# Kernel tuning notes

Hardware: AMD Instinct MI355X
Metric: run time of the kernel (lower is better)

## Reference

```python
import jax, jax.numpy as jnp
import numpy as np

DEPTH = 11  # tree depth -> depth+1 routing steps, n_nodes = 2**(DEPTH+1)-1 = 4095


def setup_inputs() -> dict:
    key = jax.random.key(0)
    k1, k2, k3 = jax.random.split(key, 3)
    B, D_in, D_out = 8192, 2048, 2048
    n_nodes = 2 ** (DEPTH + 1) - 1
    x = jax.random.normal(k1, (B, D_in), dtype=jnp.float32)
    # nn.Linear(input_width, n_nodes, bias=False).weight : (n_nodes, D_in)
    W_in = jax.random.normal(k2, (n_nodes, D_in), dtype=jnp.float32) / np.sqrt(D_in).astype(np.float32)
    # nn.Linear(n_nodes, output_width, bias=False).weight : (D_out, n_nodes)
    W_out = jax.random.normal(k3, (D_out, n_nodes), dtype=jnp.float32) / np.sqrt(n_nodes).astype(np.float32)
    return {"x": x, "W_in": W_in, "W_out": W_out}


def reference(x, W_in, W_out):
    B = x.shape[0]
    # Torch loop recomputes linear_in(x) every step; the result is identical each
    # iteration, so compute the (B, n_nodes) logits once and gather per depth step.
    logits_all = x @ W_in.T  # (B, n_nodes)

    def step(cur, _):
        # gather the logit of each sample's current tree node
        score = jnp.take_along_axis(logits_all, cur[:, None], axis=1)[:, 0]  # (B,)
        nxt = cur * 2 + (score >= 0).astype(jnp.int32) + 1  # left/right child
        return nxt, (cur, score)

    init = jnp.zeros((B,), dtype=jnp.int32)
    _, (nodes, scores) = jax.lax.scan(step, init, None, length=DEPTH + 1)
    nodes = nodes.T    # (B, depth+1) visited node ids
    scores = scores.T  # (B, depth+1) selected logits

    mlp1 = jax.nn.gelu(scores, approximate=False)  # exact GELU, matches nn.GELU
    # Conditional output projection: only the depth+1 visited columns of W_out
    # contribute per sample (FFF / conditional-MoE semantics).
    W_sel = W_out.T[nodes]  # (B, depth+1, D_out)
    return jnp.einsum('bd,bdo->bo', mlp1, W_sel)
```

## Files before the change

### kernel.cpp

```cpp
#include <hip/hip_runtime.h>
#include <math.h>

#define B_SZ     8192
#define D_IN     2048
#define D_OUT    2048
#define N_NODES  4095
#define STEPS    12
#define N_LEAVES 2048
#define N_SUB    512
#define CAP      64

__global__ __launch_bounds__(256) void transpose_wout(
    const float* __restrict__ W, float* __restrict__ Wt) {
  __shared__ float tile[64][65];
  const int bx = blockIdx.x;
  const int tid = threadIdx.x;
  const int col0 = (bx & 63) * 64;
  const int row0 = (bx >> 6) * 64;
  const int r  = tid >> 4;
  const int c4 = (tid & 15) * 4;

  #pragma unroll
  for (int i = 0; i < 4; ++i) {
    const int row = r + i * 16;
    const float* src = W + (size_t)(row0 + row) * N_NODES + col0 + c4;
    if (col0 + c4 + 3 < N_NODES) {
      const float4 v = *(const float4*)src;
      tile[c4 + 0][row] = v.x; tile[c4 + 1][row] = v.y;
      tile[c4 + 2][row] = v.z; tile[c4 + 3][row] = v.w;
    } else {
      #pragma unroll
      for (int k = 0; k < 4; ++k)
        tile[c4 + k][row] = (col0 + c4 + k < N_NODES) ? src[k] : 0.0f;
    }
  }
  __syncthreads();
  #pragma unroll
  for (int i = 0; i < 4; ++i) {
    const int rn = r + i * 16;
    const int node = col0 + rn;
    if (node < N_NODES) {
      float4 v;
      v.x = tile[rn][c4 + 0]; v.y = tile[rn][c4 + 1];
      v.z = tile[rn][c4 + 2]; v.w = tile[rn][c4 + 3];
      *(float4*)(Wt + (size_t)node * D_OUT + row0 + c4) = v;
    }
  }
}

__global__ __launch_bounds__(256) void route_kernel(
    const float* __restrict__ x, const float* __restrict__ W_in,
    int* __restrict__ cnt, int* __restrict__ bucket,
    float* __restrict__ gsc) {
  const int wave = (int)((blockIdx.x * (size_t)blockDim.x + threadIdx.x) >> 6);
  const int lane = threadIdx.x & 63;
  if (wave >= B_SZ) return;

  const float4* xr = (const float4*)(x + (size_t)wave * D_IN);
  float4 xv[8];
  #pragma unroll
  for (int i = 0; i < 8; ++i) xv[i] = xr[lane + i * 64];

  int cur = 0;
  #pragma unroll
  for (int d = 0; d < STEPS; ++d) {
    const float4* wr = (const float4*)(W_in + (size_t)cur * D_IN);
    float s = 0.0f;
    #pragma unroll
    for (int i = 0; i < 8; ++i) {
      const float4 w = wr[lane + i * 64];
      s += xv[i].x * w.x + xv[i].y * w.y + xv[i].z * w.z + xv[i].w * w.w;
    }
    #pragma unroll
    for (int off = 32; off > 0; off >>= 1) s += __shfl_xor(s, off);

    if (lane == 0) {
      gsc[wave * STEPS + d] = 0.5f * s * (1.0f + erff(s * 0.70710678118654752f));
      if (d == STEPS - 1) {
        const int leaf = cur - 2047;
        const int pos = atomicAdd(&cnt[leaf], 1);
        if (pos < CAP) bucket[leaf * CAP + pos] = wave;
      }
    }
    cur = cur * 2 + ((s >= 0.0f) ? 2 : 1);
  }
}

__global__ __launch_bounds__(64, 4) void out_kernel(
    const float* __restrict__ Wt, const int* __restrict__ cnt,
    const int* __restrict__ bucket, const float* __restrict__ gsc,
    float* __restrict__ out) {
  const int sub = blockIdx.x;
  const int col = blockIdx.y * 256 + threadIdx.x * 4;

  int anc[10];
  {
    int nd = 511 + sub;
    #pragma unroll
    for (int d = 9; d >= 0; --d) { anc[d] = nd; nd = (nd - 1) >> 1; }
  }
  const int p10a = 1023 + 2 * sub;
  const int leaf0n = 2047 + 4 * sub;

  float4 wa[10], wp[2], wl[4];
  #pragma unroll
  for (int d = 0; d < 10; ++d)
    wa[d] = *(const float4*)(Wt + (size_t)anc[d] * D_OUT + col);
  #pragma unroll
  for (int k = 0; k < 2; ++k)
    wp[k] = *(const float4*)(Wt + (size_t)(p10a + k) * D_OUT + col);
  #pragma unroll
  for (int k = 0; k < 4; ++k)
    wl[k] = *(const float4*)(Wt + (size_t)(leaf0n + k) * D_OUT + col);

  #pragma unroll
  for (int local = 0; local < 4; ++local) {
    const int leaf = 4 * sub + local;
    int n = cnt[leaf];
    if (n > CAP) n = CAP;
    const float4 w10 = wp[local >> 1];
    const float4 w11 = wl[local];
    for (int s = 0; s < n; ++s) {
      const int b = bucket[leaf * CAP + s];
      const float4* gp = (const float4*)(gsc + (size_t)b * STEPS);
      const float4 g0 = gp[0], g1 = gp[1], g2 = gp[2];
      float4 acc;
      acc.x = g0.x * wa[0].x; acc.y = g0.x * wa[0].y;
      acc.z = g0.x * wa[0].z; acc.w = g0.x * wa[0].w;
      acc.x += g0.y * wa[1].x; acc.y += g0.y * wa[1].y;
      acc.z += g0.y * wa[1].z; acc.w += g0.y * wa[1].w;
      acc.x += g0.z * wa[2].x; acc.y += g0.z * wa[2].y;
      acc.z += g0.z * wa[2].z; acc.w += g0.z * wa[2].w;
      acc.x += g0.w * wa[3].x; acc.y += g0.w * wa[3].y;
      acc.z += g0.w * wa[3].z; acc.w += g0.w * wa[3].w;
      acc.x += g1.x * wa[4].x; acc.y += g1.x * wa[4].y;
      acc.z += g1.x * wa[4].z; acc.w += g1.x * wa[4].w;
      acc.x += g1.y * wa[5].x; acc.y += g1.y * wa[5].y;
      acc.z += g1.y * wa[5].z; acc.w += g1.y * wa[5].w;
      acc.x += g1.z * wa[6].x; acc.y += g1.z * wa[6].y;
      acc.z += g1.z * wa[6].z; acc.w += g1.z * wa[6].w;
      acc.x += g1.w * wa[7].x; acc.y += g1.w * wa[7].y;
      acc.z += g1.w * wa[7].z; acc.w += g1.w * wa[7].w;
      acc.x += g2.x * wa[8].x; acc.y += g2.x * wa[8].y;
      acc.z += g2.x * wa[8].z; acc.w += g2.x * wa[8].w;
      acc.x += g2.y * wa[9].x; acc.y += g2.y * wa[9].y;
      acc.z += g2.y * wa[9].z; acc.w += g2.y * wa[9].w;
      acc.x += g2.z * w10.x;   acc.y += g2.z * w10.y;
      acc.z += g2.z * w10.z;   acc.w += g2.z * w10.w;
      acc.x += g2.w * w11.x;   acc.y += g2.w * w11.y;
      acc.z += g2.w * w11.z;   acc.w += g2.w * w11.w;
      *(float4*)(out + (size_t)b * D_OUT + col) = acc;
    }
  }
}

extern "C" void kernel_launch(void* const* d_in, const int* in_sizes, int n_in,
                              void* d_out, int out_size, void* d_ws, size_t ws_size,
                              hipStream_t stream) {
  const float* x     = (const float*)d_in[0];
  const float* W_in  = (const float*)d_in[1];
  const float* W_out = (const float*)d_in[2];
  float* out = (float*)d_out;

  char* p = (char*)d_ws;
  float* Wt     = (float*)p;  p += (size_t)N_NODES * D_OUT * sizeof(float);
  int*   cnt    = (int*)p;    p += (size_t)N_LEAVES * sizeof(int);
  int*   bucket = (int*)p;    p += (size_t)N_LEAVES * CAP * sizeof(int);
  float* gsc    = (float*)p;

  hipMemsetAsync(cnt, 0, (size_t)N_LEAVES * sizeof(int), stream);

  transpose_wout<<<dim3(2048), dim3(256), 0, stream>>>(W_out, Wt);

  route_kernel<<<dim3(B_SZ / 4), dim3(256), 0, stream>>>(
      x, W_in, cnt, bucket, gsc);

  out_kernel<<<dim3(N_SUB, 8), dim3(64), 0, stream>>>(
      Wt, cnt, bucket, gsc, out);
}
```

Baseline: 232.3 us.

## Fuse W_out transpose into routing kernel and prefetch both child rows

Merges the W_out transpose and the routing pass into one launch, with odd blocks transposing and even blocks routing, so the two independent memory-bound phases can overlap. Routing now loads both child rows of W_in one step ahead and computes both dot products, which removes the serialized load latency on the tree walk at the cost of doubling W_in reads and register pressure. Routing buffers the GELU scores and writes them as three float4 stores. The output kernel flattens the four leaf buckets into one loop, loading bucket ids cooperatively and software-pipelining the gsc loads two samples ahead.

```diff
diff --git a/kernel.cpp b/kernel.cpp
--- a/kernel.cpp
+++ b/kernel.cpp
@@ -10,88 +10,136 @@
 #define N_SUB    512
 #define CAP      64
 
-__global__ __launch_bounds__(256) void transpose_wout(
-    const float* __restrict__ W, float* __restrict__ Wt) {
-  __shared__ float tile[64][65];
-  const int bx = blockIdx.x;
-  const int tid = threadIdx.x;
-  const int col0 = (bx & 63) * 64;
-  const int row0 = (bx >> 6) * 64;
-  const int r  = tid >> 4;
-  const int c4 = (tid & 15) * 4;
-
-  #pragma unroll
-  for (int i = 0; i < 4; ++i) {
-    const int row = r + i * 16;
-    const float* src = W + (size_t)(row0 + row) * N_NODES + col0 + c4;
-    if (col0 + c4 + 3 < N_NODES) {
-      const float4 v = *(const float4*)src;
-      tile[c4 + 0][row] = v.x; tile[c4 + 1][row] = v.y;
-      tile[c4 + 2][row] = v.z; tile[c4 + 3][row] = v.w;
-    } else {
-      #pragma unroll
-      for (int k = 0; k < 4; ++k)
-        tile[c4 + k][row] = (col0 + c4 + k < N_NODES) ? src[k] : 0.0f;
-    }
-  }
-  __syncthreads();
-  #pragma unroll
-  for (int i = 0; i < 4; ++i) {
-    const int rn = r + i * 16;
-    const int node = col0 + rn;
-    if (node < N_NODES) {
-      float4 v;
-      v.x = tile[rn][c4 + 0]; v.y = tile[rn][c4 + 1];
-      v.z = tile[rn][c4 + 2]; v.w = tile[rn][c4 + 3];
-      *(float4*)(Wt + (size_t)node * D_OUT + row0 + c4) = v;
-    }
-  }
-}
-
-__global__ __launch_bounds__(256) void route_kernel(
+__global__ __launch_bounds__(256, 4) void route_tr_kernel(
     const float* __restrict__ x, const float* __restrict__ W_in,
+    const float* __restrict__ W_out, float* __restrict__ Wt,
     int* __restrict__ cnt, int* __restrict__ bucket,
     float* __restrict__ gsc) {
-  const int wave = (int)((blockIdx.x * (size_t)blockDim.x + threadIdx.x) >> 6);
-  const int lane = threadIdx.x & 63;
-  if (wave >= B_SZ) return;
+  __shared__ float tile[64][65];
+  const int tid = threadIdx.x;
+
+  if (blockIdx.x & 1) {
+    const int bx = blockIdx.x >> 1;
+    const int col0 = (bx & 63) * 64;
+    const int row0 = (bx >> 6) * 64;
+    const int r  = tid >> 4;
+    const int c4 = (tid & 15) * 4;
+    #pragma unroll
+    for (int i = 0; i < 4; ++i) {
+      const int row = r + i * 16;
+      const float* src = W_out + (size_t)(row0 + row) * N_NODES + col0 + c4;
+      if (col0 + c4 + 3 < N_NODES) {
+        const float4 v = *(const float4*)src;
+        tile[c4 + 0][row] = v.x; tile[c4 + 1][row] = v.y;
+        tile[c4 + 2][row] = v.z; tile[c4 + 3][row] = v.w;
+      } else {
+        #pragma unroll
+        for (int k = 0; k < 4; ++k)
+          tile[c4 + k][row] = (col0 + c4 + k < N_NODES) ? src[k] : 0.0f;
+      }
+    }
+    __syncthreads();
+    #pragma unroll
+    for (int i = 0; i < 4; ++i) {
+      const int rn = r + i * 16;
+      const int node = col0 + rn;
+      if (node < N_NODES) {
+        float4 v;
+        v.x = tile[rn][c4 + 0]; v.y = tile[rn][c4 + 1];
+        v.z = tile[rn][c4 + 2]; v.w = tile[rn][c4 + 3];
+        *(float4*)(Wt + (size_t)node * D_OUT + row0 + c4) = v;
+      }
+    }
+    return;
+  }
+
+  const int wave = (blockIdx.x >> 1) * 4 + (tid >> 6);
+  const int lane = tid & 63;
 
   const float4* xr = (const float4*)(x + (size_t)wave * D_IN);
   float4 xv[8];
   #pragma unroll
   for (int i = 0; i < 8; ++i) xv[i] = xr[lane + i * 64];
 
-  int cur = 0;
-  #pragma unroll
-  for (int d = 0; d < STEPS; ++d) {
-    const float4* wr = (const float4*)(W_in + (size_t)cur * D_IN);
-    float s = 0.0f;
+  float4 cl[8], cr[8];
+  {
+    const float4* p0 = (const float4*)W_in;
+    #pragma unroll
+    for (int i = 0; i < 8; ++i) cl[i] = p0[lane + i * 64];
+  }
+  float s = 0.0f;
+  #pragma unroll
+  for (int i = 0; i < 8; ++i)
+    s += xv[i].x * cl[i].x + xv[i].y * cl[i].y +
+         xv[i].z * cl[i].z + xv[i].w * cl[i].w;
+  {
+    const float4* p1 = (const float4*)(W_in + (size_t)1 * D_IN);
+    const float4* p2 = (const float4*)(W_in + (size_t)2 * D_IN);
+    #pragma unroll
+    for (int i = 0; i < 8; ++i) cl[i] = p1[lane + i * 64];
+    #pragma unroll
+    for (int i = 0; i < 8; ++i) cr[i] = p2[lane + i * 64];
+  }
+  #pragma unroll
+  for (int off = 32; off > 0; off >>= 1) s += __shfl_xor(s, off);
+
+  float gv[STEPS];
+  if (lane == 0) gv[0] = 0.5f * s * (1.0f + erff(s * 0.70710678118654752f));
+  int right = (s >= 0.0f) ? 1 : 0;
+  int cur = 1 + right;
+
+  #pragma unroll
+  for (int d = 1; d < STEPS; ++d) {
+    float sL = 0.0f, sR = 0.0f;
     #pragma unroll
     for (int i = 0; i < 8; ++i) {
-      const float4 w = wr[lane + i * 64];
-      s += xv[i].x * w.x + xv[i].y * w.y + xv[i].z * w.z + xv[i].w * w.w;
-    }
-    #pragma unroll
-    for (int off = 32; off > 0; off >>= 1) s += __shfl_xor(s, off);
-
+      sL += xv[i].x * cl[i].x + xv[i].y * cl[i].y +
+            xv[i].z * cl[i].z + xv[i].w * cl[i].w;
+      sR += xv[i].x * cr[i].x + xv[i].y * cr[i].y +
+            xv[i].z * cr[i].z + xv[i].w * cr[i].w;
+    }
+    const int curs = __builtin_amdgcn_readfirstlane(cur);
+    if (d < STEPS - 1) {
+      const float4* pl = (const float4*)(W_in + (size_t)(2 * curs + 1) * D_IN);
+      const float4* pr = (const float4*)(W_in + (size_t)(2 * curs + 2) * D_IN);
+      #pragma unroll
+      for (int i = 0; i < 8; ++i) cl[i] = pl[lane + i * 64];
+      #pragma unroll
+      for (int i = 0; i < 8; ++i) cr[i] = pr[lane + i * 64];
+    }
+    #pragma unroll
+    for (int off = 32; off > 0; off >>= 1) {
+      sL += __shfl_xor(sL, off);
+      sR += __shfl_xor(sR, off);
+    }
+    s = right ? sR : sL;
     if (lane == 0) {
-      gsc[wave * STEPS + d] = 0.5f * s * (1.0f + erff(s * 0.70710678118654752f));
+      gv[d] = 0.5f * s * (1.0f + erff(s * 0.70710678118654752f));
       if (d == STEPS - 1) {
-        const int leaf = cur - 2047;
+        const int leaf = curs - 2047;
         const int pos = atomicAdd(&cnt[leaf], 1);
         if (pos < CAP) bucket[leaf * CAP + pos] = wave;
       }
     }
-    cur = cur * 2 + ((s >= 0.0f) ? 2 : 1);
+    right = (s >= 0.0f) ? 1 : 0;
+    cur = 2 * curs + 1 + right;
+  }
+
+  if (lane == 0) {
+    float4* gp = (float4*)(gsc + (size_t)wave * STEPS);
+    gp[0] = make_float4(gv[0], gv[1], gv[2], gv[3]);
+    gp[1] = make_float4(gv[4], gv[5], gv[6], gv[7]);
+    gp[2] = make_float4(gv[8], gv[9], gv[10], gv[11]);
   }
 }
 
-__global__ __launch_bounds__(64, 4) void out_kernel(
+__global__ __launch_bounds__(64) void out_kernel(
     const float* __restrict__ Wt, const int* __restrict__ cnt,
     const int* __restrict__ bucket, const float* __restrict__ gsc,
     float* __restrict__ out) {
   const int sub = blockIdx.x;
-  const int col = blockIdx.y * 256 + threadIdx.x * 4;
+  const int lane = threadIdx.x;
+  const int col = blockIdx.y * 256 + lane * 4;
 
   int anc[10];
   {
@@ -113,43 +161,75 @@
   for (int k = 0; k < 4; ++k)
     wl[k] = *(const float4*)(Wt + (size_t)(leaf0n + k) * D_OUT + col);
 
-  #pragma unroll
-  for (int local = 0; local < 4; ++local) {
-    const int leaf = 4 * sub + local;
-    int n = cnt[leaf];
-    if (n > CAP) n = CAP;
-    const float4 w10 = wp[local >> 1];
-    const float4 w11 = wl[local];
-    for (int s = 0; s < n; ++s) {
-      const int b = bucket[leaf * CAP + s];
-      const float4* gp = (const float4*)(gsc + (size_t)b * STEPS);
-      const float4 g0 = gp[0], g1 = gp[1], g2 = gp[2];
+  int n0 = cnt[4 * sub + 0]; if (n0 > CAP) n0 = CAP;
+  int n1 = cnt[4 * sub + 1]; if (n1 > CAP) n1 = CAP;
+  int n2 = cnt[4 * sub + 2]; if (n2 > CAP) n2 = CAP;
+  int n3 = cnt[4 * sub + 3]; if (n3 > CAP) n3 = CAP;
+  const int p1 = n0, p2 = n0 + n1, p3 = n0 + n1 + n2;
+  const int total = p3 + n3;
+
+  for (int base = 0; base < total; base += 64) {
+    const int m = (total - base < 64) ? (total - base) : 64;
+    int packed = 0;
+    {
+      const int gi = base + lane;
+      if (gi < total) {
+        int lc, off;
+        if      (gi < p1) { lc = 0; off = 0;  }
+        else if (gi < p2) { lc = 1; off = p1; }
+        else if (gi < p3) { lc = 2; off = p2; }
+        else              { lc = 3; off = p3; }
+        const int b = bucket[(4 * sub + lc) * CAP + (gi - off)];
+        packed = (lc << 28) | b;
+      }
+    }
+    int pA = __shfl(packed, 0);
+    int pB = __shfl(packed, (m > 1) ? 1 : 0);
+    const float4* gA = (const float4*)(gsc + (size_t)(pA & 0x0FFFFFFF) * STEPS);
+    float4 a0 = gA[0], a1 = gA[1], a2 = gA[2];
+    const float4* gB = (const float4*)(gsc + (size_t)(pB & 0x0FFFFFFF) * STEPS);
+    float4 b0 = gB[0], b1 = gB[1], b2 = gB[2];
+
+    for (int j = 0; j < m; ++j) {
+      int jn = j + 2; if (jn >= m) jn = m - 1;
+      const int pC = __shfl(packed, jn);
+      const float4* gC = (const float4*)(gsc + (size_t)(pC & 0x0FFFFFFF) * STEPS);
+      const float4 t0 = gC[0], t1 = gC[1], t2 = gC[2];
+
+      const int b  = pA & 0x0FFFFFFF;
+      const int lc = pA >> 28;
+      const float4 w10 = (lc & 2) ? wp[1] : wp[0];
+      const float4 w11 = (lc & 2) ? ((lc & 1) ? wl[3] : wl[2])
+                                  : ((lc & 1) ? wl[1] : wl[0]);
       float4 acc;
-      acc.x = g0.x * wa[0].x; acc.y = g0.x * wa[0].y;
-      acc.z = g0.x * wa[0].z; acc.w = g0.x * wa[0].w;
-      acc.x += g0.y * wa[1].x; acc.y += g0.y * wa[1].y;
-      acc.z += g0.y * wa[1].z; acc.w += g0.y * wa[1].w;
-      acc.x += g0.z * wa[2].x; acc.y += g0.z * wa[2].y;
-      acc.z += g0.z * wa[2].z; acc.w += g0.z * wa[2].w;
-      acc.x += g0.w * wa[3].x; acc.y += g0.w * wa[3].y;
-      acc.z += g0.w * wa[3].z; acc.w += g0.w * wa[3].w;
-      acc.x += g1.x * wa[4].x; acc.y += g1.x * wa[4].y;
-      acc.z += g1.x * wa[4].z; acc.w += g1.x * wa[4].w;
-      acc.x += g1.y * wa[5].x; acc.y += g1.y * wa[5].y;
-      acc.z += g1.y * wa[5].z; acc.w += g1.y * wa[5].w;
-      acc.x += g1.z * wa[6].x; acc.y += g1.z * wa[6].y;
-      acc.z += g1.z * wa[6].z; acc.w += g1.z * wa[6].w;
-      acc.x += g1.w * wa[7].x; acc.y += g1.w * wa[7].y;
-      acc.z += g1.w * wa[7].z; acc.w += g1.w * wa[7].w;
-      acc.x += g2.x * wa[8].x; acc.y += g2.x * wa[8].y;
-      acc.z += g2.x * wa[8].z; acc.w += g2.x * wa[8].w;
-      acc.x += g2.y * wa[9].x; acc.y += g2.y * wa[9].y;
-      acc.z += g2.y * wa[9].z; acc.w += g2.y * wa[9].w;
-      acc.x += g2.z * w10.x;   acc.y += g2.z * w10.y;
-      acc.z += g2.z * w10.z;   acc.w += g2.z * w10.w;
-      acc.x += g2.w * w11.x;   acc.y += g2.w * w11.y;
-      acc.z += g2.w * w11.z;   acc.w += g2.w * w11.w;
+      acc.x = a0.x * wa[0].x; acc.y = a0.x * wa[0].y;
+      acc.z = a0.x * wa[0].z; acc.w = a0.x * wa[0].w;
+      acc.x += a0.y * wa[1].x; acc.y += a0.y * wa[1].y;
+      acc.z += a0.y * wa[1].z; acc.w += a0.y * wa[1].w;
+      acc.x += a0.z * wa[2].x; acc.y += a0.z * wa[2].y;
+      acc.z += a0.z * wa[2].z; acc.w += a0.z * wa[2].w;
+      acc.x += a0.w * wa[3].x; acc.y += a0.w * wa[3].y;
+      acc.z += a0.w * wa[3].z; acc.w += a0.w * wa[3].w;
+      acc.x += a1.x * wa[4].x; acc.y += a1.x * wa[4].y;
+      acc.z += a1.x * wa[4].z; acc.w += a1.x * wa[4].w;
+      acc.x += a1.y * wa[5].x; acc.y += a1.y * wa[5].y;
+      acc.z += a1.y * wa[5].z; acc.w += a1.y * wa[5].w;
+      acc.x += a1.z * wa[6].x; acc.y += a1.z * wa[6].y;
+      acc.z += a1.z * wa[6].z; acc.w += a1.z * wa[6].w;
+      acc.x += a1.w * wa[7].x; acc.y += a1.w * wa[7].y;
+      acc.z += a1.w * wa[7].z; acc.w += a1.w * wa[7].w;
+      acc.x += a2.x * wa[8].x; acc.y += a2.x * wa[8].y;
+      acc.z += a2.x * wa[8].z; acc.w += a2.x * wa[8].w;
+      acc.x += a2.y * wa[9].x; acc.y += a2.y * wa[9].y;
+      acc.z += a2.y * wa[9].z; acc.w += a2.y * wa[9].w;
+      acc.x += a2.z * w10.x;   acc.y += a2.z * w10.y;
+      acc.z += a2.z * w10.z;   acc.w += a2.z * w10.w;
+      acc.x += a2.w * w11.x;   acc.y += a2.w * w11.y;
+      acc.z += a2.w * w11.z;   acc.w += a2.w * w11.w;
       *(float4*)(out + (size_t)b * D_OUT + col) = acc;
+
+      pA = pB; a0 = b0; a1 = b1; a2 = b2;
+      pB = pC; b0 = t0; b1 = t1; b2 = t2;
     }
   }
 }
@@ -170,10 +250,8 @@
 
   hipMemsetAsync(cnt, 0, (size_t)N_LEAVES * sizeof(int), stream);
 
-  transpose_wout<<<dim3(2048), dim3(256), 0, stream>>>(W_out, Wt);
-
-  route_kernel<<<dim3(B_SZ / 4), dim3(256), 0, stream>>>(
-      x, W_in, cnt, bucket, gsc);
+  route_tr_kernel<<<dim3(4096), dim3(256), 0, stream>>>(
+      x, W_in, W_out, Wt, cnt, bucket, gsc);
 
   out_kernel<<<dim3(N_SUB, 8), dim3(64), 0, stream>>>(
       Wt, cnt, bucket, gsc, out);
```

After: 321.8 us. +38.6%, slower.
